# Kernel optimization log

Measured on AMD Instinct MI355X. Metric: run time of the kernel, lower is better.

## Reference

```python
import jax, jax.numpy as jnp
import numpy as np

B = 96            # batch; must equal out_features for the rank-growing matmul broadcast to type-check
IN_FEATURES = 3
OUT_FEATURES = 96
GRID_PLUS_ORDER = 5 + 3  # grid_size + spline_order


def setup_inputs() -> dict:
    key = jax.random.key(0)
    k1, k2 = jax.random.split(key)
    x = jax.random.normal(k1, (B, IN_FEATURES), dtype=jnp.float32)
    spline_weight = jax.random.normal(k2, (OUT_FEATURES, IN_FEATURES, GRID_PLUS_ORDER), dtype=jnp.float32)
    return {"x": x, "spline_weight": spline_weight}


def reference(x, spline_weight):
    # projected[b, o, j] = sum_i x[b, i] * W[o, i, j]  -> [B, out, G+k]
    projected = jnp.einsum('bi,oij->boj', x, spline_weight)
    res = projected[:, :, 0]  # [B, out]
    # Non-commutative composition: each step is an outer-product-style matmul that
    # grows the rank by one 'out' dim (numpy matmul broadcasting == torch's here).
    for i in range(1, IN_FEATURES):
        res = jnp.squeeze(jnp.matmul(res[..., None], projected[:, :, i][:, None, :]))
    return res  # [B, out, out, out] for in_features=3 with B == out
```

## Files before the change

kernel.cpp:

```cpp
#include <hip/hip_runtime.h>


#define NB 96

__global__ __launch_bounds__(256) void nckart_kernel(
    const float* __restrict__ x,
    const float* __restrict__ w,
    float* __restrict__ out)
{
    const int bm = blockIdx.x;
    const int b  = bm / NB;
    const int m  = bm % NB;
    const int t  = threadIdx.x;

    __shared__ float p1[NB];
    __shared__ float sp[NB];

    const float xb0 = x[b*3 + 0], xb1 = x[b*3 + 1], xb2 = x[b*3 + 2];

    if (t < NB) {
        p1[t] = xb0 * w[t*24 + 0*8 + 1]
              + xb1 * w[t*24 + 1*8 + 1]
              + xb2 * w[t*24 + 2*8 + 1];
    } else if (t < 2*NB) {
        const int p = t - NB;
        const float xm0 = x[m*3 + 0], xm1 = x[m*3 + 1], xm2 = x[m*3 + 2];
        const float s = xb0 * w[m*24 + 0*8 + 0]
                      + xb1 * w[m*24 + 1*8 + 0]
                      + xb2 * w[m*24 + 2*8 + 0];
        const float p2 = xm0 * w[p*24 + 0*8 + 2]
                       + xm1 * w[p*24 + 1*8 + 2]
                       + xm2 * w[p*24 + 2*8 + 2];
        sp[p] = s * p2;
    }
    __syncthreads();

    float4* out4 = reinterpret_cast<float4*>(out + (size_t)bm * (NB * NB));
    const float4* sp4 = reinterpret_cast<const float4*>(sp);

    #pragma unroll
    for (int it = 0; it < 9; ++it) {
        const int idx = t + it * 256;
        const int n   = idx / 24;
        const int p4  = idx % 24;
        float4 v = sp4[p4];
        const float a = p1[n];
        v.x *= a; v.y *= a; v.z *= a; v.w *= a;
        out4[idx] = v;
    }
}

extern "C" void kernel_launch(void* const* d_in, const int* in_sizes, int n_in,
                              void* d_out, int out_size, void* d_ws, size_t ws_size,
                              hipStream_t stream) {
    const float* x = (const float*)d_in[0];
    const float* w = (const float*)d_in[1];
    float* out = (float*)d_out;

    const int grid = NB * NB;
    nckart_kernel<<<grid, 256, 0, stream>>>(x, w, out);
}
```

Before: 66.23 us.

## Precompute projection tables in a prep kernel and drop shared-memory sync

New measurement: 69.49 us. 1.05x slower.

```diff
diff --git a/kernel.cpp b/kernel.cpp
--- a/kernel.cpp
+++ b/kernel.cpp
@@ -2,10 +2,28 @@
 
 
 #define NB 96
+#define TBL (NB * NB)
 
-__global__ __launch_bounds__(256) void nckart_kernel(
+typedef float f32x4 __attribute__((ext_vector_type(4)));
+
+__global__ __launch_bounds__(256) void prep_kernel(
     const float* __restrict__ x,
     const float* __restrict__ w,
+    float* __restrict__ ws)
+{
+    const int v = blockIdx.x * 256 + threadIdx.x;
+    if (v >= 3 * TBL) return;
+    const int which = v / TBL;
+    const int r     = v % TBL;
+    const int a     = r / NB;
+    const int c     = r % NB;
+    const float x0 = x[a*3 + 0], x1 = x[a*3 + 1], x2 = x[a*3 + 2];
+    const int j = which;
+    ws[v] = x0 * w[c*24 + 0*8 + j] + x1 * w[c*24 + 1*8 + j] + x2 * w[c*24 + 2*8 + j];
+}
+
+__global__ __launch_bounds__(256) void nckart_store(
+    const float* __restrict__ ws,
     float* __restrict__ out)
 {
     const int bm = blockIdx.x;
@@ -13,40 +31,21 @@
     const int m  = bm % NB;
     const int t  = threadIdx.x;
 
-    __shared__ float p1[NB];
-    __shared__ float sp[NB];
+    const float*  s  = ws;
+    const float*  p1 = ws + TBL;
+    const f32x4*  q4 = reinterpret_cast<const f32x4*>(ws + 2 * TBL);
 
-    const float xb0 = x[b*3 + 0], xb1 = x[b*3 + 1], xb2 = x[b*3 + 2];
-
-    if (t < NB) {
-        p1[t] = xb0 * w[t*24 + 0*8 + 1]
-              + xb1 * w[t*24 + 1*8 + 1]
-              + xb2 * w[t*24 + 2*8 + 1];
-    } else if (t < 2*NB) {
-        const int p = t - NB;
-        const float xm0 = x[m*3 + 0], xm1 = x[m*3 + 1], xm2 = x[m*3 + 2];
-        const float s = xb0 * w[m*24 + 0*8 + 0]
-                      + xb1 * w[m*24 + 1*8 + 0]
-                      + xb2 * w[m*24 + 2*8 + 0];
-        const float p2 = xm0 * w[p*24 + 0*8 + 2]
-                       + xm1 * w[p*24 + 1*8 + 2]
-                       + xm2 * w[p*24 + 2*8 + 2];
-        sp[p] = s * p2;
-    }
-    __syncthreads();
-
-    float4* out4 = reinterpret_cast<float4*>(out + (size_t)bm * (NB * NB));
-    const float4* sp4 = reinterpret_cast<const float4*>(sp);
+    const float A = s[bm];
+    f32x4* o4 = reinterpret_cast<f32x4*>(out) + (size_t)bm * (NB * NB / 4);
 
     #pragma unroll
     for (int it = 0; it < 9; ++it) {
         const int idx = t + it * 256;
         const int n   = idx / 24;
         const int p4  = idx % 24;
-        float4 v = sp4[p4];
-        const float a = p1[n];
-        v.x *= a; v.y *= a; v.z *= a; v.w *= a;
-        out4[idx] = v;
+        f32x4 v = q4[m * 24 + p4];
+        v *= (A * p1[b * NB + n]);
+        o4[idx] = v;
     }
 }
 
@@ -56,7 +55,8 @@
     const float* x = (const float*)d_in[0];
     const float* w = (const float*)d_in[1];
     float* out = (float*)d_out;
+    float* ws  = (float*)d_ws;
 
-    const int grid = NB * NB;
-    nckart_kernel<<<grid, 256, 0, stream>>>(x, w, out);
+    prep_kernel<<<(3 * TBL + 255) / 256, 256, 0, stream>>>(x, w, ws);
+    nckart_store<<<TBL, 256, 0, stream>>>(ws, out);
 }
```
